# Optimization experiments

Hardware: AMD Instinct MI355X
Metric: run time of the kernel (lower is better)

Reference implementation:

```python
import jax, jax.numpy as jnp
import numpy as np
from jax import lax

NPOINT = 1024
K = 32
GN_GROUPS = 32
EPS = 1e-5


def farthest_point_sample(xyz, npoint):
    # xyz: (B,N,3) -> idx (B,npoint). Deterministic start at index 0.
    B, N, _ = xyz.shape
    dist0 = jnp.full((B, N), 1e10, dtype=xyz.dtype)
    far0 = jnp.zeros((B,), dtype=jnp.int32)
    barange = jnp.arange(B)

    def step(carry, _):
        dist, far = carry
        centroid = xyz[barange, far][:, None, :]              # (B,1,3)
        d = jnp.sum((xyz - centroid) ** 2, axis=-1)           # (B,N)
        dist = jnp.minimum(dist, d)
        far_new = jnp.argmax(dist, axis=-1).astype(jnp.int32)
        return (dist, far_new), far

    _, idxs = lax.scan(step, (dist0, far0), None, length=npoint)
    return idxs.T  # (B,npoint)


def conv1x1(x, w, b):
    # x: (B,Cin,M,K), w: (Cout,Cin)
    return jnp.einsum('oc,bcmk->bomk', w, x) + b[None, :, None, None]


def group_norm(x, gamma, beta, groups):
    B, C, M, Kk = x.shape
    xg = x.reshape(B, groups, C // groups, M, Kk)
    mu = xg.mean(axis=(2, 3, 4), keepdims=True)
    var = xg.var(axis=(2, 3, 4), keepdims=True)
    xg = (xg - mu) * lax.rsqrt(var + EPS)
    x = xg.reshape(B, C, M, Kk)
    return x * gamma[None, :, None, None] + beta[None, :, None, None]


def setup_inputs() -> dict:
    key = jax.random.key(0)
    ks = jax.random.split(key, 4)
    B, N, Cin = 16, 8192, 64
    hid, out_ch, in_total = 64, 128, 3 + Cin
    return {
        'xyz': jax.random.normal(ks[0], (B, N, 3), jnp.float32),
        'feat': jax.random.normal(ks[1], (B, N, Cin), jnp.float32),
        'w1': jax.random.normal(ks[2], (hid, in_total), jnp.float32) * 0.1,
        'b1': jnp.zeros((hid,), jnp.float32),
        'g1w': jnp.ones((hid,), jnp.float32),
        'g1b': jnp.zeros((hid,), jnp.float32),
        'w2': jax.random.normal(ks[3], (out_ch, hid), jnp.float32) * 0.1,
        'b2': jnp.zeros((out_ch,), jnp.float32),
        'g2w': jnp.ones((out_ch,), jnp.float32),
        'g2b': jnp.zeros((out_ch,), jnp.float32),
    }


def reference(xyz, feat, w1, b1, g1w, g1b, w2, b2, g2w, g2b):
    B, N, _ = xyz.shape
    M = min(NPOINT, N)
    k = min(K, N)

    fps_idx = farthest_point_sample(lax.stop_gradient(xyz), M)   # (B,M) ints
    batch = jnp.arange(B)[:, None]
    centroids = xyz[batch, fps_idx]                              # (B,M,3)

    # kNN via squared distances (same ordering as cdist p=2)
    d2 = (jnp.sum(centroids ** 2, -1)[:, :, None]
          + jnp.sum(xyz ** 2, -1)[:, None, :]
          - 2.0 * jnp.einsum('bmd,bnd->bmn', centroids, xyz))    # (B,M,N)
    knn_idx = lax.top_k(-d2, k)[1]                               # (B,M,k)

    b3 = jnp.arange(B)[:, None, None]
    group_xyz = xyz[b3, knn_idx]                                 # (B,M,k,3)
    delta = group_xyz - centroids[:, :, None, :]
    gfeat = feat[b3, knn_idx]                                    # (B,M,k,Cin)
    gf = jnp.concatenate([delta, gfeat], axis=-1)                # (B,M,k,3+Cin)
    x = jnp.transpose(gf, (0, 3, 1, 2))                          # (B,C,M,k)

    x = jax.nn.relu(group_norm(conv1x1(x, w1, b1), g1w, g1b, GN_GROUPS))
    x = jax.nn.relu(group_norm(conv1x1(x, w2, b2), g2w, g2b, GN_GROUPS))
    out = jnp.max(x, axis=-1)                                    # (B,out_ch,M)
    new_feat = jnp.transpose(out, (0, 2, 1))                     # (B,M,out_ch)
    return (centroids, new_feat)
```

## Files before the change

kernel.cpp:

```cpp
#include <hip/hip_runtime.h>
#include <cstdint>

#define BB 16
#define NN 8192
#define MM 1024
#define KNN 32
#define CIN 64
#define HID 64
#define OCH 128

#define KNN_OFF   0u
#define SUM1_OFF  524288u
#define SUM2_OFF  526336u
#define A1_OFF    530432u
#define D1_OFF    531456u
#define A2_OFF    532480u
#define D2_OFF    534528u
#define W2B_OFF   536576u
#define W1B_OFF   540672u
#define Y1_OFF    543744u
#define PTS4_OFF  Y1_OFF

typedef unsigned long long u64;
typedef float f32x4 __attribute__((ext_vector_type(4)));
typedef float f32x2 __attribute__((ext_vector_type(2)));
typedef short bf16x8 __attribute__((ext_vector_type(8)));

__device__ __forceinline__ unsigned short f2bf(float f) {
  union { float f; unsigned u; } v; v.f = f;
  unsigned r = v.u + 0x7FFFu + ((v.u >> 16) & 1u);
  return (unsigned short)(r >> 16);
}

__global__ __launch_bounds__(256) void k0_init(const float* __restrict__ xyz,
                                               const float* __restrict__ w1,
                                               const float* __restrict__ w2,
                                               float* __restrict__ ws) {
  int t = blockIdx.x * 256 + threadIdx.x;
  if (t < 12288) ws[SUM1_OFF + t] = 0.0f;
  if (t < 4096) {
    unsigned lo = f2bf(w2[2 * t]);
    unsigned hi = f2bf(w2[2 * t + 1]);
    ((unsigned*)(ws + W2B_OFF))[t] = lo | (hi << 16);
  }
  if (t < 6144) {
    int n = t / 96, kk = t % 96;
    float val = 0.0f;
    if (kk < 3) val = w1[n * 67 + kk];
    else if (kk >= 4 && kk < 68) val = w1[n * 67 + kk - 1];
    ((unsigned short*)(ws + W1B_OFF))[t] = f2bf(val);
  }
  if (t < BB * NN) {
    #pragma clang fp contract(off)
    float x = xyz[(size_t)t * 3], y = xyz[(size_t)t * 3 + 1], z = xyz[(size_t)t * 3 + 2];
    ((float4*)(ws + PTS4_OFF))[t] = make_float4(x, y, z, (x * x + y * y) + z * z);
  }
}

__device__ __forceinline__ u64 wave_max_u64(u64 v) {
  #define DPP_RND(ctrl, rm)                                                     \
  {                                                                             \
    int lo_ = __builtin_amdgcn_update_dpp(0, (int)(unsigned)(v & 0xFFFFFFFFull),\
                                          ctrl, rm, 0xf, true);                 \
    int hi_ = __builtin_amdgcn_update_dpp(0, (int)(unsigned)(v >> 32),          \
                                          ctrl, rm, 0xf, true);                 \
    u64 o_ = ((u64)(unsigned)hi_ << 32) | (unsigned)lo_;                        \
    v = o_ > v ? o_ : v;                                                        \
  }
  DPP_RND(0x111, 0xf)
  DPP_RND(0x112, 0xf)
  DPP_RND(0x114, 0xf)
  DPP_RND(0x118, 0xf)
  DPP_RND(0x142, 0xa)
  DPP_RND(0x143, 0xc)
  #undef DPP_RND
  return v;
}

__global__ __launch_bounds__(256) void fps_kernel(const float* __restrict__ xyz,
                                                  float* __restrict__ cent) {
  #pragma clang fp contract(off)
  __shared__ float4 sp4[NN];
  __shared__ u64 slots[MM];
  const int b = blockIdx.x, tid = threadIdx.x;
  const float* xp = xyz + (size_t)b * NN * 3;
  f32x2 px[16], py[16], pz[16];
  float dist0[16], dist1[16];
  #pragma unroll
  for (int i = 0; i < 16; ++i) {
    int n0 = tid + (2 * i) * 256, n1 = tid + (2 * i + 1) * 256;
    float x0 = xp[n0 * 3], y0 = xp[n0 * 3 + 1], z0 = xp[n0 * 3 + 2];
    float x1 = xp[n1 * 3], y1 = xp[n1 * 3 + 1], z1 = xp[n1 * 3 + 2];
    px[i] = (f32x2){x0, x1}; py[i] = (f32x2){y0, y1}; pz[i] = (f32x2){z0, z1};
    sp4[n0] = make_float4(x0, y0, z0, 0.0f);
    sp4[n1] = make_float4(x1, y1, z1, 0.0f);
    dist0[i] = 1e10f; dist1[i] = 1e10f;
  }
  for (int s = tid; s < MM; s += 256) slots[s] = 0ull;
  __syncthreads();
  int far = 0;
  float* co = cent + (size_t)b * MM * 3;
  for (int step = 0; step < MM; ++step) {
    float4 c4 = sp4[far];
    if (tid == 0) { co[step * 3] = c4.x; co[step * 3 + 1] = c4.y; co[step * 3 + 2] = c4.z; }
    f32x2 cx = (f32x2){c4.x, c4.x}, cy = (f32x2){c4.y, c4.y}, cz = (f32x2){c4.z, c4.z};
    float best = -1.0f; int bi = 0;
    #pragma unroll
    for (int i = 0; i < 16; ++i) {
      f32x2 dx = px[i] - cx, dy = py[i] - cy, dz = pz[i] - cz;
      f32x2 d = (dx * dx + dy * dy) + dz * dz;
      float dm0 = fminf(dist0[i], d.x);
      float dm1 = fminf(dist1[i], d.y);
      dist0[i] = dm0; dist1[i] = dm1;
      if (dm0 > best) { best = dm0; bi = tid + (2 * i) * 256; }
      if (dm1 > best) { best = dm1; bi = tid + (2 * i + 1) * 256; }
    }
    u64 key = ((u64)__float_as_uint(best) << 32) | (unsigned)(8191 - bi);
    key = wave_max_u64(key);
    if ((tid & 63) == 63) atomicMax(&slots[step], key);
    __syncthreads();
    far = 8191 - (int)(unsigned)(slots[step] & 0xFFFFFFFFull);
  }
}

__global__ __launch_bounds__(512) void knn_kernel(const float4* __restrict__ pts4,
                                                  const float* __restrict__ cent,
                                                  int* __restrict__ knnout) {
  #pragma clang fp contract(off)
  __shared__ __align__(16) char smem[65536];
  unsigned* blo = (unsigned*)smem;
  unsigned* bhi = (unsigned*)(smem + 32768);
  u64* marea = (u64*)smem;
  const int tid = threadIdx.x;
  const int lane = tid & 63;
  const int w = tid >> 6;
  const int b = blockIdx.x >> 4;
  const int m = ((blockIdx.x & 15) << 6) + lane;
  const float* cp = cent + ((size_t)b * MM + m) * 3;
  float cx = cp[0], cy = cp[1], cz = cp[2];
  float cn2 = (cx * cx + cy * cy) + cz * cz;
  u64 key[32];
  {
    u64 initk = ((u64)(__float_as_uint(3e38f) ^ 0x80000000u) << 32) | 0xFFFFFFFFull;
    #pragma unroll
    for (int j = 0; j < 32; ++j) key[j] = initk;
  }
  float kthf = 3e38f;

  auto insert = [&](u64 cand) {
    bool cprev = false; u64 kprev = 0;
    #pragma unroll
    for (int j = 0; j < 32; ++j) {
      bool cj = cand < key[j];
      u64 cur = key[j];
      u64 nv = cj ? cand : cur;
      key[j] = cprev ? kprev : nv;
      cprev = cj; kprev = cur;
    }
    unsigned hb = (unsigned)(key[31] >> 32);
    unsigned ob = (hb & 0x80000000u) ? (hb ^ 0x80000000u) : ~hb;
    kthf = __uint_as_float(ob);
  };

  int cnt = 0;
  auto flush = [&]() {
    int mc = cnt;
    #pragma unroll
    for (int off = 1; off < 64; off <<= 1) { int o = __shfl_xor(mc, off); mc = o > mc ? o : mc; }
    for (int i = 0; i < mc; ++i) {
      u64 cand = ((u64)bhi[i * 512 + tid] << 32) | blo[i * 512 + tid];
      if (i < cnt && cand < key[31]) insert(cand);
    }
    cnt = 0;
  };

  const int nbase = __builtin_amdgcn_readfirstlane(w * 1024);
  const float4* pb = pts4 + (size_t)b * NN + nbase;
  for (int n0 = 0; n0 < 1024; n0 += 8) {
    #pragma unroll
    for (int j = 0; j < 8; ++j) {
      int n = n0 + j;
      float4 p = pb[n];
      float dot = fmaf(cz, p.z, fmaf(cy, p.y, cx * p.x));
      float d2 = (cn2 + p.w) - 2.0f * dot;
      if (d2 <= kthf) {
        unsigned db = __float_as_uint(d2);
        unsigned fk = db ^ (((int)db < 0) ? 0xFFFFFFFFu : 0x80000000u);
        blo[cnt * 512 + tid] = (unsigned)(nbase + n);
        bhi[cnt * 512 + tid] = fk;
        cnt++;
      }
    }
    if (__ballot(cnt >= 9)) flush();
  }
  flush();
  __syncthreads();

  auto publish = [&](int a) {
    u64* ap = marea + a * 2048;
    #pragma unroll
    for (int j = 0; j < 32; ++j) ap[j * 64 + lane] = key[j];
  };
  auto merge_from = [&](int a) {
    u64* ap = marea + a * 2048;
    for (int j = 0; j < 32; ++j) {
      u64 cand = ap[j * 64 + lane];
      if (cand < key[31]) insert(cand);
    }
  };
  if (w & 1) publish(w >> 1);
  __syncthreads();
  if (!(w & 1)) merge_from(w >> 1);
  __syncthreads();
  if (w == 2) publish(0);
  if (w == 6) publish(1);
  __syncthreads();
  if (w == 0) merge_from(0);
  if (w == 4) merge_from(1);
  __syncthreads();
  if (w == 4) publish(0);
  __syncthreads();
  if (w == 0) {
    merge_from(0);
    int* op = knnout + ((size_t)b * MM + m) * KNN;
    #pragma unroll
    for (int j = 0; j < 32; ++j) op[j] = (int)(key[j] & 0xFFFFFFFFull);
  }
}

__global__ __launch_bounds__(256) void conv1_kernel(const float* __restrict__ xyz,
                                                    const float* __restrict__ feat,
                                                    const float* __restrict__ cent,
                                                    const int* __restrict__ knn,
                                                    const unsigned short* __restrict__ w1b,
                                                    const float* __restrict__ b1,
                                                    float* __restrict__ y1) {
  __shared__ __align__(16) unsigned short gsm[4][32 * 104];
  const int tid = threadIdx.x, lane = tid & 63, w = tid >> 6;
  const int wid = blockIdx.x * 4 + w;
  const int b = wid >> 10;
  unsigned short* gf = gsm[w];

  int idxv = 0;
  if (lane < 32) idxv = knn[(size_t)wid * 32 + lane];

  {
    int row = lane >> 1, h = (lane & 1) * 16;
    ushort4 z4 = {0, 0, 0, 0};
    *(ushort4*)(gf + row * 104 + 64 + h + 0)  = z4;
    *(ushort4*)(gf + row * 104 + 64 + h + 4)  = z4;
    *(ushort4*)(gf + row * 104 + 64 + h + 8)  = z4;
    *(ushort4*)(gf + row * 104 + 64 + h + 12) = z4;
  }
  const float* cp = cent + (size_t)wid * 3;
  float ccx = cp[0], ccy = cp[1], ccz = cp[2];
  if (lane < 32) {
    const float* pp = xyz + ((size_t)b * NN + idxv) * 3;
    ushort4 dv;
    dv.x = f2bf(pp[0] - ccx); dv.y = f2bf(pp[1] - ccy); dv.z = f2bf(pp[2] - ccz);
    dv.w = 0;
    *(ushort4*)(gf + lane * 104) = dv;
  }
  const float4* fb = (const float4*)feat;
  #pragma unroll
  for (int i = 0; i < 8; ++i) {
    int v = i * 64 + lane;
    int row = v >> 4, part = v & 15;
    int ridx = __shfl(idxv, row);
    float4 f4 = fb[(size_t)(b * NN + ridx) * 16 + part];
    ushort4 s;
    s.x = f2bf(f4.x); s.y = f2bf(f4.y); s.z = f2bf(f4.z); s.w = f2bf(f4.w);
    *(ushort4*)(gf + row * 104 + 4 + part * 4) = s;
  }
  __builtin_amdgcn_s_waitcnt(0);
  __builtin_amdgcn_wave_barrier();

  const int quad = lane >> 4, lr = lane & 15;
  bf16x8 bw[4][3];
  float b1v[4];
  #pragma unroll
  for (int nt = 0; nt < 4; ++nt) {
    #pragma unroll
    for (int ks = 0; ks < 3; ++ks)
      bw[nt][ks] = *(const bf16x8*)(w1b + (size_t)(nt * 16 + lr) * 96 + ks * 32 + quad * 8);
    b1v[nt] = b1[nt * 16 + lr];
  }
  f32x4 acc[2][4];
  #pragma unroll
  for (int mt = 0; mt < 2; ++mt)
    #pragma unroll
    for (int nt = 0; nt < 4; ++nt)
      acc[mt][nt] = (f32x4){0.f, 0.f, 0.f, 0.f};
  #pragma unroll
  for (int ks = 0; ks < 3; ++ks) {
    bf16x8 a0 = *(const bf16x8*)(gf + (0 + lr) * 104 + ks * 32 + quad * 8);
    bf16x8 a1 = *(const bf16x8*)(gf + (16 + lr) * 104 + ks * 32 + quad * 8);
    #pragma unroll
    for (int nt = 0; nt < 4; ++nt) {
      acc[0][nt] = __builtin_amdgcn_mfma_f32_16x16x32_bf16(a0, bw[nt][ks], acc[0][nt], 0, 0, 0);
      acc[1][nt] = __builtin_amdgcn_mfma_f32_16x16x32_bf16(a1, bw[nt][ks], acc[1][nt], 0, 0, 0);
    }
  }
  float* yo = y1 + (size_t)wid * 2048;
  #pragma unroll
  for (int mt = 0; mt < 2; ++mt)
    #pragma unroll
    for (int rg = 0; rg < 4; ++rg) {
      int row = mt * 16 + quad * 4 + rg;
      #pragma unroll
      for (int nt = 0; nt < 4; ++nt)
        yo[row * 64 + nt * 16 + lr] = acc[mt][nt][rg] + b1v[nt];
    }
}

__global__ __launch_bounds__(256) void red1_kernel(const float* __restrict__ y1,
                                                   float* __restrict__ sums1) {
  __shared__ float acc[128];
  int tid = threadIdx.x;
  if (tid < 128) acc[tid] = 0.0f;
  __syncthreads();
  const float4* yp = (const float4*)(y1 + (size_t)blockIdx.x * 65536);
  int c0 = (4 * tid) & 63;
  float s0 = 0, s1 = 0, s2 = 0, s3 = 0, q0 = 0, q1 = 0, q2 = 0, q3 = 0;
  for (int it = 0; it < 64; ++it) {
    float4 v = yp[it * 256 + tid];
    s0 += v.x; q0 = fmaf(v.x, v.x, q0);
    s1 += v.y; q1 = fmaf(v.y, v.y, q1);
    s2 += v.z; q2 = fmaf(v.z, v.z, q2);
    s3 += v.w; q3 = fmaf(v.w, v.w, q3);
  }
  atomicAdd(&acc[c0], s0); atomicAdd(&acc[c0 + 1], s1);
  atomicAdd(&acc[c0 + 2], s2); atomicAdd(&acc[c0 + 3], s3);
  atomicAdd(&acc[64 + c0], q0); atomicAdd(&acc[64 + c0 + 1], q1);
  atomicAdd(&acc[64 + c0 + 2], q2); atomicAdd(&acc[64 + c0 + 3], q3);
  __syncthreads();
  if (tid < 128) {
    int b = blockIdx.x >> 5;
    atomicAdd(&sums1[b * 128 + tid], acc[tid]);
  }
}

__global__ void coeffs_kernel(const float* __restrict__ sums,
                              const float* __restrict__ gamma,
                              const float* __restrict__ beta,
                              float* __restrict__ a, float* __restrict__ d,
                              int nch, int cpg, float invn) {
  int t = blockIdx.x * blockDim.x + threadIdx.x;
  if (t >= BB * nch) return;
  int b = t / nch, c = t % nch, g = c / cpg;
  float S = 0, Q = 0;
  for (int j = 0; j < cpg; ++j) {
    S += sums[b * 2 * nch + g * cpg + j];
    Q += sums[b * 2 * nch + nch + g * cpg + j];
  }
  float mu = S * invn;
  float var = Q * invn - mu * mu;
  float rs = 1.0f / sqrtf(var + 1e-5f);
  float ga = gamma[c];
  a[t] = rs * ga;
  d[t] = beta[c] - mu * rs * ga;
}

struct Conv2Frag {
  bf16x8 bfr[8][2];
  float  b2v[8];
};

__device__ __forceinline__ void load_w2_frags(const unsigned short* __restrict__ w2b,
                                              const float* __restrict__ b2,
                                              int lane, Conv2Frag& F) {
  const int quad = lane >> 4, lr = lane & 15;
  #pragma unroll
  for (int nt = 0; nt < 8; ++nt) {
    #pragma unroll
    for (int t = 0; t < 2; ++t)
      F.bfr[nt][t] = *(const bf16x8*)(w2b + (size_t)(nt * 16 + lr) * 64 + t * 32 + quad * 8);
    F.b2v[nt] = b2[nt * 16 + lr];
  }
}

__device__ __forceinline__ void conv2_wave_mfma(const float* __restrict__ y1,
                                                const float* __restrict__ a1,
                                                const float* __restrict__ d1,
                                                unsigned short* __restrict__ hrow,
                                                int wid, int b, int lane,
                                                const Conv2Frag& F,
                                                f32x4 acc[2][8]) {
  const int quad = lane >> 4, lr = lane & 15;
  const int r = lane >> 1, c0 = (lane & 1) * 32;
  const float4* yrow = (const float4*)(y1 + (size_t)wid * 2048 + r * 64 + c0);
  const float4* ap = (const float4*)(a1 + b * 64 + c0);
  const float4* dp = (const float4*)(d1 + b * 64 + c0);
  #pragma unroll
  for (int g = 0; g < 8; ++g) {
    float4 v = yrow[g];
    float4 av = ap[g & 7], dv = dp[g & 7];
    ushort4 sv;
    sv.x = f2bf(fmaxf(0.0f, fmaf(v.x, av.x, dv.x)));
    sv.y = f2bf(fmaxf(0.0f, fmaf(v.y, av.y, dv.y)));
    sv.z = f2bf(fmaxf(0.0f, fmaf(v.z, av.z, dv.z)));
    sv.w = f2bf(fmaxf(0.0f, fmaf(v.w, av.w, dv.w)));
    *(ushort4*)(hrow + r * 72 + c0 + 4 * g) = sv;
  }
  __builtin_amdgcn_s_waitcnt(0);
  __builtin_amdgcn_wave_barrier();
  #pragma unroll
  for (int mt = 0; mt < 2; ++mt)
    #pragma unroll
    for (int nt = 0; nt < 8; ++nt)
      acc[mt][nt] = (f32x4){0.f, 0.f, 0.f, 0.f};
  #pragma unroll
  for (int t = 0; t < 2; ++t) {
    bf16x8 a0 = *(const bf16x8*)(hrow + (0 + lr) * 72 + t * 32 + quad * 8);
    bf16x8 a1f = *(const bf16x8*)(hrow + (16 + lr) * 72 + t * 32 + quad * 8);
    #pragma unroll
    for (int nt = 0; nt < 8; ++nt) {
      acc[0][nt] = __builtin_amdgcn_mfma_f32_16x16x32_bf16(a0,  F.bfr[nt][t], acc[0][nt], 0, 0, 0);
      acc[1][nt] = __builtin_amdgcn_mfma_f32_16x16x32_bf16(a1f, F.bfr[nt][t], acc[1][nt], 0, 0, 0);
    }
  }
}

__global__ __launch_bounds__(256) void conv2_stats_kernel(const float* __restrict__ y1,
                                                          const float* __restrict__ a1,
                                                          const float* __restrict__ d1,
                                                          const unsigned short* __restrict__ w2b,
                                                          const float* __restrict__ b2,
                                                          float* __restrict__ sums2) {
  __shared__ __align__(16) unsigned short hsm[4][32 * 72];
  __shared__ float sacc[128], qacc[128];
  const int tid = threadIdx.x, lane = tid & 63, w = tid >> 6;
  const int wid = blockIdx.x * 4 + w;
  const int b = blockIdx.x >> 8;
  if (tid < 128) { sacc[tid] = 0.0f; qacc[tid] = 0.0f; }
  __syncthreads();
  Conv2Frag F;
  load_w2_frags(w2b, b2, lane, F);
  f32x4 acc[2][8];
  conv2_wave_mfma(y1, a1, d1, hsm[w], wid, b, lane, F, acc);
  const int lr = lane & 15;
  #pragma unroll
  for (int nt = 0; nt < 8; ++nt) {
    float s = 0, q = 0;
    #pragma unroll
    for (int mt = 0; mt < 2; ++mt)
      #pragma unroll
      for (int rg = 0; rg < 4; ++rg) {
        float z = acc[mt][nt][rg] + F.b2v[nt];
        s += z; q = fmaf(z, z, q);
      }
    atomicAdd(&sacc[nt * 16 + lr], s);
    atomicAdd(&qacc[nt * 16 + lr], q);
  }
  __syncthreads();
  if (tid < 128) {
    atomicAdd(&sums2[b * 256 + tid], sacc[tid]);
    atomicAdd(&sums2[b * 256 + 128 + tid], qacc[tid]);
  }
}

__global__ __launch_bounds__(256) void final_kernel(const float* __restrict__ y1,
                                                    const float* __restrict__ a1,
                                                    const float* __restrict__ d1,
                                                    const unsigned short* __restrict__ w2b,
                                                    const float* __restrict__ b2,
                                                    const float* __restrict__ a2,
                                                    const float* __restrict__ d2,
                                                    float* __restrict__ nf) {
  __shared__ __align__(16) unsigned short hsm[4][32 * 72];
  const int tid = threadIdx.x, lane = tid & 63, w = tid >> 6;
  const int wid = blockIdx.x * 4 + w;
  const int b = blockIdx.x >> 8;
  Conv2Frag F;
  load_w2_frags(w2b, b2, lane, F);
  f32x4 acc[2][8];
  conv2_wave_mfma(y1, a1, d1, hsm[w], wid, b, lane, F, acc);
  const int lr = lane & 15;
  float az[8], dz[8];
  #pragma unroll
  for (int nt = 0; nt < 8; ++nt) {
    az[nt] = a2[b * 128 + nt * 16 + lr];
    dz[nt] = d2[b * 128 + nt * 16 + lr];
  }
  float pmax[8];
  #pragma unroll
  for (int nt = 0; nt < 8; ++nt) {
    float mx = -3e38f;
    #pragma unroll
    for (int mt = 0; mt < 2; ++mt)
      #pragma unroll
      for (int rg = 0; rg < 4; ++rg) {
        float z = acc[mt][nt][rg] + F.b2v[nt];
        float v = fmaxf(0.0f, fmaf(z, az[nt], dz[nt]));
        mx = fmaxf(mx, v);
      }
    mx = fmaxf(mx, __shfl_xor(mx, 16));
    mx = fmaxf(mx, __shfl_xor(mx, 32));
    pmax[nt] = mx;
  }
  if (lane < 16) {
    float* op = nf + (size_t)wid * 128;
    #pragma unroll
    for (int nt = 0; nt < 8; ++nt) op[nt * 16 + lr] = pmax[nt];
  }
}

extern "C" void kernel_launch(void* const* d_in, const int* in_sizes, int n_in,
                              void* d_out, int out_size, void* d_ws, size_t ws_size,
                              hipStream_t stream) {
  const float* xyz  = (const float*)d_in[0];
  const float* feat = (const float*)d_in[1];
  const float* w1   = (const float*)d_in[2];
  const float* b1   = (const float*)d_in[3];
  const float* g1w  = (const float*)d_in[4];
  const float* g1b  = (const float*)d_in[5];
  const float* w2   = (const float*)d_in[6];
  const float* b2   = (const float*)d_in[7];
  const float* g2w  = (const float*)d_in[8];
  const float* g2b  = (const float*)d_in[9];
  float* ws = (float*)d_ws;
  float* cent = (float*)d_out;
  float* nf   = (float*)d_out + BB * MM * 3;
  const float4* pts4 = (const float4*)(ws + PTS4_OFF);
  int*   knn   = (int*)(ws + KNN_OFF);
  float* sums1 = ws + SUM1_OFF;
  float* sums2 = ws + SUM2_OFF;
  float* a1 = ws + A1_OFF; float* d1 = ws + D1_OFF;
  float* a2 = ws + A2_OFF; float* d2 = ws + D2_OFF;
  const unsigned short* w2b = (const unsigned short*)(ws + W2B_OFF);
  const unsigned short* w1b = (const unsigned short*)(ws + W1B_OFF);
  float* y1 = ws + Y1_OFF;

  hipLaunchKernelGGL(k0_init, dim3(512), dim3(256), 0, stream, xyz, w1, w2, ws);
  hipLaunchKernelGGL(fps_kernel, dim3(16), dim3(256), 0, stream, xyz, cent);
  hipLaunchKernelGGL(knn_kernel, dim3(256), dim3(512), 0, stream, pts4, cent, knn);
  hipLaunchKernelGGL(conv1_kernel, dim3(4096), dim3(256), 0, stream,
                     xyz, feat, cent, knn, w1b, b1, y1);
  hipLaunchKernelGGL(red1_kernel, dim3(512), dim3(256), 0, stream, y1, sums1);
  hipLaunchKernelGGL(coeffs_kernel, dim3(4), dim3(256), 0, stream,
                     sums1, g1w, g1b, a1, d1, 64, 2, 1.0f / 65536.0f);
  hipLaunchKernelGGL(conv2_stats_kernel, dim3(4096), dim3(256), 0, stream,
                     y1, a1, d1, w2b, b2, sums2);
  hipLaunchKernelGGL(coeffs_kernel, dim3(8), dim3(256), 0, stream,
                     sums2, g2w, g2b, a2, d2, 128, 4, 1.0f / 131072.0f);
  hipLaunchKernelGGL(final_kernel, dim3(4096), dim3(256), 0, stream,
                     y1, a1, d1, w2b, b2, a2, d2, nf);
}
```

Measured before the change: 1.567 ms.

## Fuse GroupNorm-1 statistics into conv1 and defer FPS centroid writes

```diff
diff --git a/kernel.cpp b/kernel.cpp
--- a/kernel.cpp
+++ b/kernel.cpp
@@ -99,10 +99,8 @@
   for (int s = tid; s < MM; s += 256) slots[s] = 0ull;
   __syncthreads();
   int far = 0;
-  float* co = cent + (size_t)b * MM * 3;
   for (int step = 0; step < MM; ++step) {
     float4 c4 = sp4[far];
-    if (tid == 0) { co[step * 3] = c4.x; co[step * 3 + 1] = c4.y; co[step * 3 + 2] = c4.z; }
     f32x2 cx = (f32x2){c4.x, c4.x}, cy = (f32x2){c4.y, c4.y}, cz = (f32x2){c4.z, c4.z};
     float best = -1.0f; int bi = 0;
     #pragma unroll
@@ -120,6 +118,12 @@
     if ((tid & 63) == 63) atomicMax(&slots[step], key);
     __syncthreads();
     far = 8191 - (int)(unsigned)(slots[step] & 0xFFFFFFFFull);
+  }
+  float* co = cent + (size_t)b * MM * 3;
+  for (int s = tid; s < MM; s += 256) {
+    int fs = (s == 0) ? 0 : (8191 - (int)(unsigned)(slots[s - 1] & 0xFFFFFFFFull));
+    float4 c = sp4[fs];
+    co[s * 3 + 0] = c.x; co[s * 3 + 1] = c.y; co[s * 3 + 2] = c.z;
   }
 }
 
@@ -234,12 +238,17 @@
                                                     const int* __restrict__ knn,
                                                     const unsigned short* __restrict__ w1b,
                                                     const float* __restrict__ b1,
-                                                    float* __restrict__ y1) {
+                                                    float* __restrict__ y1,
+                                                    float* __restrict__ sums1) {
   __shared__ __align__(16) unsigned short gsm[4][32 * 104];
+  __shared__ float s1acc[64], q1acc[64];
   const int tid = threadIdx.x, lane = tid & 63, w = tid >> 6;
   const int wid = blockIdx.x * 4 + w;
   const int b = wid >> 10;
   unsigned short* gf = gsm[w];
+
+  if (tid < 64) { s1acc[tid] = 0.0f; q1acc[tid] = 0.0f; }
+  __syncthreads();
 
   int idxv = 0;
   if (lane < 32) idxv = knn[(size_t)wid * 32 + lane];
@@ -302,41 +311,35 @@
     }
   }
   float* yo = y1 + (size_t)wid * 2048;
+  float s_nt[4] = {0.f, 0.f, 0.f, 0.f};
+  float q_nt[4] = {0.f, 0.f, 0.f, 0.f};
   #pragma unroll
   for (int mt = 0; mt < 2; ++mt)
     #pragma unroll
     for (int rg = 0; rg < 4; ++rg) {
       int row = mt * 16 + quad * 4 + rg;
       #pragma unroll
-      for (int nt = 0; nt < 4; ++nt)
-        yo[row * 64 + nt * 16 + lr] = acc[mt][nt][rg] + b1v[nt];
-    }
-}
-
-__global__ __launch_bounds__(256) void red1_kernel(const float* __restrict__ y1,
-                                                   float* __restrict__ sums1) {
-  __shared__ float acc[128];
-  int tid = threadIdx.x;
-  if (tid < 128) acc[tid] = 0.0f;
-  __syncthreads();
-  const float4* yp = (const float4*)(y1 + (size_t)blockIdx.x * 65536);
-  int c0 = (4 * tid) & 63;
-  float s0 = 0, s1 = 0, s2 = 0, s3 = 0, q0 = 0, q1 = 0, q2 = 0, q3 = 0;
-  for (int it = 0; it < 64; ++it) {
-    float4 v = yp[it * 256 + tid];
-    s0 += v.x; q0 = fmaf(v.x, v.x, q0);
-    s1 += v.y; q1 = fmaf(v.y, v.y, q1);
-    s2 += v.z; q2 = fmaf(v.z, v.z, q2);
-    s3 += v.w; q3 = fmaf(v.w, v.w, q3);
-  }
-  atomicAdd(&acc[c0], s0); atomicAdd(&acc[c0 + 1], s1);
-  atomicAdd(&acc[c0 + 2], s2); atomicAdd(&acc[c0 + 3], s3);
-  atomicAdd(&acc[64 + c0], q0); atomicAdd(&acc[64 + c0 + 1], q1);
-  atomicAdd(&acc[64 + c0 + 2], q2); atomicAdd(&acc[64 + c0 + 3], q3);
-  __syncthreads();
-  if (tid < 128) {
-    int b = blockIdx.x >> 5;
-    atomicAdd(&sums1[b * 128 + tid], acc[tid]);
+      for (int nt = 0; nt < 4; ++nt) {
+        float z = acc[mt][nt][rg] + b1v[nt];
+        yo[row * 64 + nt * 16 + lr] = z;
+        s_nt[nt] += z;
+        q_nt[nt] = fmaf(z, z, q_nt[nt]);
+      }
+    }
+  #pragma unroll
+  for (int nt = 0; nt < 4; ++nt) {
+    float s = s_nt[nt], q = q_nt[nt];
+    s += __shfl_xor(s, 16); s += __shfl_xor(s, 32);
+    q += __shfl_xor(q, 16); q += __shfl_xor(q, 32);
+    if (quad == 0) {
+      atomicAdd(&s1acc[nt * 16 + lr], s);
+      atomicAdd(&q1acc[nt * 16 + lr], q);
+    }
+  }
+  __syncthreads();
+  if (tid < 64) {
+    atomicAdd(&sums1[b * 128 + tid], s1acc[tid]);
+    atomicAdd(&sums1[b * 128 + 64 + tid], q1acc[tid]);
   }
 }
 
@@ -535,8 +538,7 @@
   hipLaunchKernelGGL(fps_kernel, dim3(16), dim3(256), 0, stream, xyz, cent);
   hipLaunchKernelGGL(knn_kernel, dim3(256), dim3(512), 0, stream, pts4, cent, knn);
   hipLaunchKernelGGL(conv1_kernel, dim3(4096), dim3(256), 0, stream,
-                     xyz, feat, cent, knn, w1b, b1, y1);
-  hipLaunchKernelGGL(red1_kernel, dim3(512), dim3(256), 0, stream, y1, sums1);
+                     xyz, feat, cent, knn, w1b, b1, y1, sums1);
   hipLaunchKernelGGL(coeffs_kernel, dim3(4), dim3(256), 0, stream,
                      sums1, g1w, g1b, a1, d1, 64, 2, 1.0f / 65536.0f);
   hipLaunchKernelGGL(conv2_stats_kernel, dim3(4096), dim3(256), 0, stream,
```

Measured after the change: 1.548 ms. No clear change (-1.2%).
